# Optimization experiments

Hardware: AMD Instinct MI355X
Metric: run time of the kernel (lower is better)

## Reference

```python
import jax, jax.numpy as jnp
import numpy as np

SCALE = 8.0  # (dim // n_heads) ** 0.5 = (1024 // 16) ** 0.5


def setup_inputs() -> dict:
    key = jax.random.key(0)
    kq, kk, kv = jax.random.split(key, 3)
    shape = (2, 16, 2048, 64)  # [B, H, N, Dh]
    q = jax.random.normal(kq, shape, dtype=jnp.float32)
    k = jax.random.normal(kk, shape, dtype=jnp.float32)
    v = jax.random.normal(kv, shape, dtype=jnp.float32)
    return {"q": q, "k": k, "v": v}


def reference(q, k, v):
    # scores[b,h,n,m] = sum_d q[b,h,n,d] * k[b,h,m,d], then MULTIPLIED by scale
    # (the original multiplies by sqrt(head_dim), it does not divide).
    scores = jnp.einsum('bhnd,bhmd->bhnm', q, k) * SCALE
    scores = jax.nn.softmax(scores, axis=-1)
    # Faithful to the original quirky einsum: sums over n (query axis), keeps m.
    # out[b,h,m,d] = (sum_n scores[b,h,n,m]) * v[b,h,m,d]
    out = jnp.einsum('bhnm,bhmd->bhmd', scores, v)
    return out
```

## Files before the change

kernel.cpp:

```cpp
#include <hip/hip_runtime.h>
#include <math.h>

#define BH 32
#define NN 2048
#define DD 64
#define BHNN (BH * NN)
#define QK ((size_t)BH * NN * DD)

#define QSCALE 11.5415603f

typedef __attribute__((ext_vector_type(8)))  _Float16 halfx8;
typedef __attribute__((ext_vector_type(4)))  _Float16 halfx4;
typedef __attribute__((ext_vector_type(16))) float    floatx16;

__device__ inline float fexp2(float x) { return __builtin_amdgcn_exp2f(x); }
__device__ inline float flog2(float x) { return __builtin_amdgcn_logf(x); }

__device__ inline int rowmap(int r, int half) {
    return (r & 3) + 8 * (r >> 2) + 4 * half;
}

__global__ __launch_bounds__(256) void convert_kernel(const float4* __restrict__ q,
                                                      const float4* __restrict__ k,
                                                      _Float16* __restrict__ qhi,
                                                      _Float16* __restrict__ khi) {
    size_t gid = (size_t)blockIdx.x * 256 + threadIdx.x;
    float4 qa = q[gid];
    float4 ka = k[gid];
    float qf[4] = {qa.x, qa.y, qa.z, qa.w};
    float kf[4] = {ka.x, ka.y, ka.z, ka.w};
    halfx4 h, kh;
#pragma unroll
    for (int i = 0; i < 4; ++i) {
        h[i]  = (_Float16)(qf[i] * QSCALE);
        kh[i] = (_Float16)kf[i];
    }
    *(halfx4*)&qhi[gid * 4] = h;
    size_t rowbase = (gid * 4) & ~(size_t)63;
    int j = (int)((gid >> 1) & 7) ^ (int)((gid >> 4) & 7);
    *(halfx4*)&khi[rowbase + (size_t)(j << 3) + ((gid & 1) << 2)] = kh;
}

__device__ inline void stage_tile_async4(const _Float16* __restrict__ gtile,
                                         _Float16* lds, int wave, int lane) {
#pragma unroll
    for (int i = 0; i < 4; ++i) {
        const char* gp = (const char*)gtile + wave * 4096 + i * 1024 + lane * 16;
        char* lp = (char*)lds + wave * 4096 + i * 1024;
        __builtin_amdgcn_global_load_lds(
            (const __attribute__((address_space(1))) unsigned int*)gp,
            (__attribute__((address_space(3))) unsigned int*)lp, 16, 0, 0);
    }
}
__device__ inline void stage_tile_async8(const _Float16* __restrict__ gtile,
                                         _Float16* lds, int wave, int lane) {
#pragma unroll
    for (int i = 0; i < 2; ++i) {
        const char* gp = (const char*)gtile + wave * 2048 + i * 1024 + lane * 16;
        char* lp = (char*)lds + wave * 2048 + i * 1024;
        __builtin_amdgcn_global_load_lds(
            (const __attribute__((address_space(1))) unsigned int*)gp,
            (__attribute__((address_space(3))) unsigned int*)lp, 16, 0, 0);
    }
}

__device__ inline void load_a(const _Float16* __restrict__ qhi_row,
                              int half, halfx8 ah[4]) {
#pragma unroll
    for (int ks = 0; ks < 4; ++ks)
        ah[ks] = *(const halfx8*)&qhi_row[ks * 16 + half * 8];
}

__global__ __launch_bounds__(256, 4) void stats_kernel(const _Float16* __restrict__ qhi,
                                                       const _Float16* __restrict__ khi,
                                                       float* __restrict__ smax_p,
                                                       float* __restrict__ sden_p) {
    __shared__ _Float16 K2[2 * 128 * 64];
    const int g    = blockIdx.x & 63;
    const int bh   = g & 31;
    const int ms   = g >> 5;
    const int n0   = (blockIdx.x >> 6) * 128;
    const int tid  = threadIdx.x;
    const int wave = tid >> 6, lane = tid & 63;
    const int half = lane >> 5, l31 = lane & 31;
    const int xr   = l31 & 7;
    const size_t base = (size_t)bh * NN * DD;

    const _Float16* khi_b = khi + base;
    stage_tile_async4(khi_b + (size_t)(ms * 8) * 8192, K2, wave, lane);

    halfx8 ah[4];
    {
        size_t ro = base + (size_t)(n0 + wave * 32 + l31) * DD;
        load_a(qhi + ro, half, ah);
    }

    float m_run[16], d_run[16];
#pragma unroll
    for (int r = 0; r < 16; ++r) { m_run[r] = -INFINITY; d_run[r] = 0.f; }

    __syncthreads();

#pragma unroll 1
    for (int mti = 0; mti < 8; ++mti) {
        const _Float16* Kc = K2 + (mti & 1) * 8192;
        if (mti < 7)
            stage_tile_async4(khi_b + (size_t)(ms * 8 + mti + 1) * 8192,
                              K2 + ((mti + 1) & 1) * 8192, wave, lane);

#pragma unroll 1
        for (int p = 0; p < 2; ++p) {
            floatx16 acc[2];
#pragma unroll
            for (int t = 0; t < 2; ++t)
#pragma unroll
                for (int e = 0; e < 16; ++e) acc[t][e] = 0.f;

#pragma unroll
            for (int tt = 0; tt < 2; ++tt) {
                const int mr = (p * 2 + tt) * 32 + l31;
                const _Float16* rowp = Kc + (size_t)mr * 64;
#pragma unroll
                for (int ks = 0; ks < 4; ++ks) {
                    const int j = (ks * 2 + half) ^ xr;
                    halfx8 bhf = *(const halfx8*)&rowp[j << 3];
                    acc[tt] = __builtin_amdgcn_mfma_f32_32x32x16_f16(ah[ks], bhf, acc[tt], 0, 0, 0);
                }
            }

#pragma unroll
            for (int r = 0; r < 16; ++r) {
                float tmax = fmaxf(acc[0][r], acc[1][r]);
                float m_new = fmaxf(m_run[r], tmax);
                float s = fexp2(acc[0][r] - m_new) + fexp2(acc[1][r] - m_new);
                d_run[r] = d_run[r] * fexp2(m_run[r] - m_new) + s;
                m_run[r] = m_new;
            }
        }

        if (mti < 7) __syncthreads();
    }

    float* smp = smax_p + ((size_t)ms * BH + bh) * NN;
    float* sdp = sden_p + ((size_t)ms * BH + bh) * NN;
#pragma unroll
    for (int r = 0; r < 16; ++r) {
        float M = m_run[r];
#pragma unroll
        for (int off = 1; off < 32; off <<= 1)
            M = fmaxf(M, __shfl_xor(M, off));
        float dd = d_run[r] * fexp2(m_run[r] - M);
#pragma unroll
        for (int off = 1; off < 32; off <<= 1)
            dd += __shfl_xor(dd, off);
        if (l31 == 0) {
            int row = n0 + wave * 32 + rowmap(r, half);
            smp[row] = M;
            sdp[row] = dd;
        }
    }
}

__global__ __launch_bounds__(512, 4) void wsum_kernel(const _Float16* __restrict__ qhi,
                                                      const _Float16* __restrict__ khi,
                                                      const float* __restrict__ smax_p,
                                                      const float* __restrict__ sden_p,
                                                      const float* __restrict__ v,
                                                      float* __restrict__ out) {
    __shared__ _Float16 Khi[128 * 64];
    __shared__ float Ms[2048];
    __shared__ float wred[8 * 128];
    __shared__ float wfin[128];
    const int b    = blockIdx.x;
    const int bh   = b & 31;
    const int m0   = (b >> 5) * 128;
    const int tid  = threadIdx.x;
    const int wave = tid >> 6, lane = tid & 63;
    const int half = lane >> 5, l31 = lane & 31;
    const int xr   = l31 & 7;
    const size_t base = (size_t)bh * NN * DD;

    stage_tile_async8(khi + base + (size_t)m0 * 64, Khi, wave, lane);

    {
        size_t roff = (size_t)bh * NN + tid * 4;
        float4 m0v = *(const float4*)&smax_p[roff];
        float4 m1v = *(const float4*)&smax_p[(size_t)BHNN + roff];
        float4 d0v = *(const float4*)&sden_p[roff];
        float4 d1v = *(const float4*)&sden_p[(size_t)BHNN + roff];
        float mm0[4] = {m0v.x, m0v.y, m0v.z, m0v.w};
        float mm1[4] = {m1v.x, m1v.y, m1v.z, m1v.w};
        float dd0[4] = {d0v.x, d0v.y, d0v.z, d0v.w};
        float dd1[4] = {d1v.x, d1v.y, d1v.z, d1v.w};
#pragma unroll
        for (int j = 0; j < 4; ++j) {
            float M = fmaxf(mm0[j], mm1[j]);
            float den = dd0[j] * fexp2(mm0[j] - M) + dd1[j] * fexp2(mm1[j] - M);
            Ms[tid * 4 + j] = M + flog2(den);
        }
    }
    __syncthreads();

    float wacc0 = 0.f, wacc1 = 0.f, wacc2 = 0.f, wacc3 = 0.f;

#pragma unroll 1
    for (int it = 0; it < 8; ++it) {
        const int ls = wave + it * 8;
        halfx8 ah[4];
        {
            size_t ro = base + (size_t)(ls * 32 + l31) * DD;
            load_a(qhi + ro, half, ah);
        }

#pragma unroll 1
        for (int p = 0; p < 2; ++p) {
            floatx16 acc[2];
#pragma unroll
            for (int t = 0; t < 2; ++t)
#pragma unroll
                for (int e = 0; e < 16; ++e) acc[t][e] = 0.f;

#pragma unroll
            for (int tt = 0; tt < 2; ++tt) {
                const int mr = (p * 2 + tt) * 32 + l31;
                const _Float16* rowp = Khi + (size_t)mr * 64;
#pragma unroll
                for (int ks = 0; ks < 4; ++ks) {
                    const int j = (ks * 2 + half) ^ xr;
                    halfx8 bhf = *(const halfx8*)&rowp[j << 3];
                    acc[tt] = __builtin_amdgcn_mfma_f32_32x32x16_f16(ah[ks], bhf, acc[tt], 0, 0, 0);
                }
            }

            float w0 = 0.f, w1 = 0.f;
#pragma unroll
            for (int r = 0; r < 16; ++r) {
                const int lrow = ls * 32 + rowmap(r, half);
                float Madj = Ms[lrow];
                w0 += fexp2(acc[0][r] - Madj);
                w1 += fexp2(acc[1][r] - Madj);
            }
            if (p == 0) { wacc0 += w0; wacc1 += w1; }
            else        { wacc2 += w0; wacc3 += w1; }
        }
    }

    float wacc[4] = {wacc0, wacc1, wacc2, wacc3};
#pragma unroll
    for (int t = 0; t < 4; ++t) wacc[t] += __shfl_xor(wacc[t], 32);
    if (half == 0) {
#pragma unroll
        for (int t = 0; t < 4; ++t) wred[wave * 128 + t * 32 + l31] = wacc[t];
    }
    __syncthreads();
    if (tid < 128) {
        float s = 0.f;
#pragma unroll
        for (int w = 0; w < 8; ++w) s += wred[w * 128 + tid];
        wfin[tid] = s;
    }
    __syncthreads();

    const float4* v4 = (const float4*)(v + base + (size_t)m0 * DD);
    float4* o4 = (float4*)(out + base + (size_t)m0 * DD);
#pragma unroll
    for (int i = 0; i < 4; ++i) {
        int idx = tid + 512 * i;
        float ww = wfin[idx >> 4];
        float4 vv = v4[idx];
        o4[idx] = make_float4(vv.x * ww, vv.y * ww, vv.z * ww, vv.w * ww);
    }
}

extern "C" void kernel_launch(void* const* d_in, const int* in_sizes, int n_in,
                              void* d_out, int out_size, void* d_ws, size_t ws_size,
                              hipStream_t stream) {
    const float* q = (const float*)d_in[0];
    const float* k = (const float*)d_in[1];
    const float* v = (const float*)d_in[2];
    float* out = (float*)d_out;

    _Float16* qhi = (_Float16*)d_ws;
    _Float16* khi = qhi + QK;
    float* smax_p = (float*)(khi + QK);
    float* sden_p = smax_p + 2 * BHNN;

    convert_kernel<<<QK / 4 / 256, 256, 0, stream>>>((const float4*)q, (const float4*)k,
                                                     qhi, khi);
    stats_kernel<<<1024, 256, 0, stream>>>(qhi, khi, smax_p, sden_p);
    wsum_kernel<<<512, 512, 0, stream>>>(qhi, khi, smax_p, sden_p, v, out);
}
```

Baseline: 159.5 us.

## Share K tiles across twice as many query rows in stats kernel; prefetch V

The stats kernel now runs 512-thread blocks whose eight waves cover two separate 128-row query groups. Each staged K tile in LDS is therefore reused by twice as many query rows, and the grid shrinks to 512 blocks. This halves global-to-LDS K staging traffic and per-block setup. The wsum kernel also issues its V loads before the cross-wave weight reduction, so that load latency overlaps the reduction and barriers. The wider block under the same 4-blocks launch bound tightens the register budget and could cause spills in the stats kernel.

```diff
diff --git a/kernel.cpp b/kernel.cpp
--- a/kernel.cpp
+++ b/kernel.cpp
@@ -41,17 +41,6 @@
     *(halfx4*)&khi[rowbase + (size_t)(j << 3) + ((gid & 1) << 2)] = kh;
 }
 
-__device__ inline void stage_tile_async4(const _Float16* __restrict__ gtile,
-                                         _Float16* lds, int wave, int lane) {
-#pragma unroll
-    for (int i = 0; i < 4; ++i) {
-        const char* gp = (const char*)gtile + wave * 4096 + i * 1024 + lane * 16;
-        char* lp = (char*)lds + wave * 4096 + i * 1024;
-        __builtin_amdgcn_global_load_lds(
-            (const __attribute__((address_space(1))) unsigned int*)gp,
-            (__attribute__((address_space(3))) unsigned int*)lp, 16, 0, 0);
-    }
-}
 __device__ inline void stage_tile_async8(const _Float16* __restrict__ gtile,
                                          _Float16* lds, int wave, int lane) {
 #pragma unroll
@@ -71,27 +60,29 @@
         ah[ks] = *(const halfx8*)&qhi_row[ks * 16 + half * 8];
 }
 
-__global__ __launch_bounds__(256, 4) void stats_kernel(const _Float16* __restrict__ qhi,
+__global__ __launch_bounds__(512, 4) void stats_kernel(const _Float16* __restrict__ qhi,
                                                        const _Float16* __restrict__ khi,
                                                        float* __restrict__ smax_p,
                                                        float* __restrict__ sden_p) {
     __shared__ _Float16 K2[2 * 128 * 64];
-    const int g    = blockIdx.x & 63;
+    const int b    = blockIdx.x;
+    const int g    = b & 63;
     const int bh   = g & 31;
     const int ms   = g >> 5;
-    const int n0   = (blockIdx.x >> 6) * 128;
+    const int n0   = (b >> 6) * 128;
     const int tid  = threadIdx.x;
     const int wave = tid >> 6, lane = tid & 63;
     const int half = lane >> 5, l31 = lane & 31;
     const int xr   = l31 & 7;
+    const int sub  = wave >> 2, w4 = wave & 3;
     const size_t base = (size_t)bh * NN * DD;
 
     const _Float16* khi_b = khi + base;
-    stage_tile_async4(khi_b + (size_t)(ms * 8) * 8192, K2, wave, lane);
+    stage_tile_async8(khi_b + (size_t)(ms * 8) * 8192, K2, wave, lane);
 
     halfx8 ah[4];
     {
-        size_t ro = base + (size_t)(n0 + wave * 32 + l31) * DD;
+        size_t ro = base + (size_t)(n0 + sub * 1024 + w4 * 32 + l31) * DD;
         load_a(qhi + ro, half, ah);
     }
 
@@ -105,7 +96,7 @@
     for (int mti = 0; mti < 8; ++mti) {
         const _Float16* Kc = K2 + (mti & 1) * 8192;
         if (mti < 7)
-            stage_tile_async4(khi_b + (size_t)(ms * 8 + mti + 1) * 8192,
+            stage_tile_async8(khi_b + (size_t)(ms * 8 + mti + 1) * 8192,
                               K2 + ((mti + 1) & 1) * 8192, wave, lane);
 
 #pragma unroll 1
@@ -154,7 +145,7 @@
         for (int off = 1; off < 32; off <<= 1)
             dd += __shfl_xor(dd, off);
         if (l31 == 0) {
-            int row = n0 + wave * 32 + rowmap(r, half);
+            int row = n0 + sub * 1024 + w4 * 32 + rowmap(r, half);
             smp[row] = M;
             sdp[row] = dd;
         }
@@ -245,6 +236,11 @@
         }
     }
 
+    const float4* v4 = (const float4*)(v + base + (size_t)m0 * DD);
+    float4 vpre[4];
+#pragma unroll
+    for (int i = 0; i < 4; ++i) vpre[i] = v4[tid + 512 * i];
+
     float wacc[4] = {wacc0, wacc1, wacc2, wacc3};
 #pragma unroll
     for (int t = 0; t < 4; ++t) wacc[t] += __shfl_xor(wacc[t], 32);
@@ -261,14 +257,13 @@
     }
     __syncthreads();
 
-    const float4* v4 = (const float4*)(v + base + (size_t)m0 * DD);
     float4* o4 = (float4*)(out + base + (size_t)m0 * DD);
 #pragma unroll
     for (int i = 0; i < 4; ++i) {
         int idx = tid + 512 * i;
         float ww = wfin[idx >> 4];
-        float4 vv = v4[idx];
-        o4[idx] = make_float4(vv.x * ww, vv.y * ww, vv.z * ww, vv.w * ww);
+        o4[idx] = make_float4(vpre[i].x * ww, vpre[i].y * ww,
+                              vpre[i].z * ww, vpre[i].w * ww);
     }
 }
 
@@ -287,6 +282,6 @@
 
     convert_kernel<<<QK / 4 / 256, 256, 0, stream>>>((const float4*)q, (const float4*)k,
                                                      qhi, khi);
-    stats_kernel<<<1024, 256, 0, stream>>>(qhi, khi, smax_p, sden_p);
+    stats_kernel<<<512, 512, 0, stream>>>(qhi, khi, smax_p, sden_p);
     wsum_kernel<<<512, 512, 0, stream>>>(qhi, khi, smax_p, sden_p, v, out);
 }
```

After: 159.5 us. About the same (-0.0%).
